# Optimization experiments

Measured on AMD Instinct MI355X. Metric: run time of the kernel, lower is better.

## Reference

```python
import jax, jax.numpy as jnp
import numpy as np

B, N, D_MODEL = 8, 1024, 512
H, DK = 8, 64
STATIONS = 128
MASK_NEG = -1e9
LN_EPS = 1e-6


def setup_inputs() -> dict:
    key = jax.random.key(0)
    ks = jax.random.split(key, 9)
    return {
        "hidden_states": jax.random.normal(ks[0], (B, N, D_MODEL), dtype=jnp.float32),
        "rpe": jax.random.normal(ks[1], (B, H, N, N), dtype=jnp.float32) * 0.1,
        "Wq": jax.random.normal(ks[2], (H * DK, D_MODEL), dtype=jnp.float32) * 0.02,
        "Wk": jax.random.normal(ks[3], (H * DK, D_MODEL), dtype=jnp.float32) * 0.02,
        "Wv": jax.random.normal(ks[4], (H * DK, D_MODEL), dtype=jnp.float32) * 0.02,
        "fc_w": jax.random.normal(ks[5], (D_MODEL, H * DK), dtype=jnp.float32) * 0.02,
        "fc_b": jnp.zeros((D_MODEL,), dtype=jnp.float32),
        "ln_g": jnp.ones((D_MODEL,), dtype=jnp.float32),
        "ln_b": jnp.zeros((D_MODEL,), dtype=jnp.float32),
    }


def _star_mask(n, stations):
    # q_k_mask: query i attends to key j iff j < stations or i == j
    idx = jnp.arange(n)
    return (idx[None, :] < stations) | (idx[:, None] == idx[None, :])  # [n, n] bool


def reference(hidden_states, rpe, Wq, Wk, Wv, fc_w, fc_b, ln_g, ln_b):
    b, n, _ = hidden_states.shape
    residual = hidden_states
    q = (hidden_states @ Wq.T).reshape(b, n, H, DK)
    k = (hidden_states @ Wk.T).reshape(b, n, H, DK)
    v = (hidden_states @ Wv.T).reshape(b, n, H, DK)
    # sparse star+self-loop QK^T with inline RPE add (dense emulation of QKP_mm_tvm)
    scores = jnp.einsum("bihd,bjhd->bhij", q, k) + rpe  # [b,h,n,n]
    mask = _star_mask(n, STATIONS)
    scores = jnp.where(mask[None, None], scores, MASK_NEG)
    scores = scores / jnp.sqrt(jnp.float32(DK))
    attn = jax.nn.softmax(scores, axis=-1)
    # AttnV_mm_tvm: sparse attn-weights times V
    ctx = jnp.einsum("bhij,bjhd->bihd", attn, v).reshape(b, n, H * DK)
    ctx = ctx @ fc_w.T + fc_b + residual
    mu = jnp.mean(ctx, axis=-1, keepdims=True)
    var = jnp.var(ctx, axis=-1, keepdims=True)
    return (ctx - mu) / jnp.sqrt(var + LN_EPS) * ln_g + ln_b
```

## Files before the change

kernel.cpp:

```cpp
#include <hip/hip_runtime.h>
#include <hip/hip_bf16.h>
#include <math.h>

#define B_  8
#define N_  1024
#define DM  512
#define H_  8
#define DK_ 64
#define ST  128

typedef __attribute__((ext_vector_type(8))) short short8;
typedef __attribute__((ext_vector_type(4))) float floatx4;

#define GLD16(gp, lp)                                                          \
    __builtin_amdgcn_global_load_lds(                                          \
        (const __attribute__((address_space(1))) void*)(gp),                   \
        (__attribute__((address_space(3))) void*)(lp), 16, 0, 0)

__device__ __forceinline__ float b2f(short u) {
    union { unsigned int i; float f; } c;
    c.i = ((unsigned int)(unsigned short)u) << 16;
    return c.f;
}
__device__ __forceinline__ unsigned short f2b(float f) {
    __hip_bfloat16 t = __float2bfloat16(f);
    return *(unsigned short*)&t;
}

struct CastArgs {
    const float* src[5];
    unsigned short* dst[5];
    int n[5];
};

__global__ __launch_bounds__(256)
void cast_bf16_kernel(CastArgs a)
{
    const int j = blockIdx.y;
    const float* __restrict__ s = a.src[j];
    unsigned short* __restrict__ d = a.dst[j];
    const int n = a.n[j];
    int i = (blockIdx.x * 256 + threadIdx.x) * 8;
    if (i >= n) return;
    float4 x0 = *(const float4*)&s[i];
    float4 x1 = *(const float4*)&s[i + 4];
    ushort4 o0, o1;
    o0.x = f2b(x0.x); o0.y = f2b(x0.y); o0.z = f2b(x0.z); o0.w = f2b(x0.w);
    o1.x = f2b(x1.x); o1.y = f2b(x1.y); o1.z = f2b(x1.z); o1.w = f2b(x1.w);
    *(ushort4*)&d[i] = o0;
    *(ushort4*)&d[i + 4] = o1;
}

__device__ __forceinline__
void gemm_core(const unsigned short* __restrict__ A,
               const unsigned short* __restrict__ W,
               int m0, int n0, unsigned short* As, unsigned short* Bs,
               floatx4 acc[4][4])
{
    const int tid = threadIdx.x;
    const int lane = tid & 63;
    const int wave = tid >> 6;
    const int wm = wave >> 1, wn = wave & 1;
    const int srow = tid >> 2;
    const int skq  = (tid & 3) * 8;
    const unsigned short* Ag = A + (size_t)(m0 + srow) * 512 + skq;
    const unsigned short* Bg = W + (size_t)(n0 + srow) * 512 + skq;
    const int mrow = lane & 15;
    const int koff = (lane >> 4) * 8;

    for (int kt = 0; kt < 512; kt += 32) {
        __syncthreads();
        GLD16(Ag + kt,            &As[tid * 8]);
        GLD16(Ag + 64 * 512 + kt, &As[2048 + tid * 8]);
        GLD16(Bg + kt,            &Bs[tid * 8]);
        GLD16(Bg + 64 * 512 + kt, &Bs[2048 + tid * 8]);
        __syncthreads();
        short8 af[4], bf[4];
        #pragma unroll
        for (int t = 0; t < 4; ++t) {
            af[t] = *(const short8*)&As[(wm * 64 + t * 16 + mrow) * 32 + koff];
            bf[t] = *(const short8*)&Bs[(wn * 64 + t * 16 + mrow) * 32 + koff];
        }
        #pragma unroll
        for (int mt = 0; mt < 4; ++mt)
            #pragma unroll
            for (int nt = 0; nt < 4; ++nt)
                acc[mt][nt] = __builtin_amdgcn_mfma_f32_16x16x32_bf16(
                    af[mt], bf[nt], acc[mt][nt], 0, 0, 0);
    }
}

__global__ __launch_bounds__(256)
void qkv_gemm_kernel(const unsigned short* __restrict__ A,
                     const unsigned short* __restrict__ W0,
                     const unsigned short* __restrict__ W1,
                     const unsigned short* __restrict__ W2,
                     unsigned short* __restrict__ qo,
                     unsigned short* __restrict__ ko,
                     unsigned short* __restrict__ vto)
{
    __shared__ __align__(16) unsigned short As[128 * 32];
    __shared__ __align__(16) unsigned short Bs[128 * 32];
    const int by = blockIdx.y;
    const int sel = by >> 2;
    const unsigned short* W = (sel == 0) ? W0 : (sel == 1 ? W1 : W2);
    const int m0 = blockIdx.x * 128;
    const int n0 = (by & 3) * 128;

    floatx4 acc[4][4];
    #pragma unroll
    for (int i = 0; i < 4; ++i)
        #pragma unroll
        for (int j = 0; j < 4; ++j)
            acc[i][j] = (floatx4){0.f, 0.f, 0.f, 0.f};

    gemm_core(A, W, m0, n0, As, Bs, acc);

    const int lane = threadIdx.x & 63;
    const int wave = threadIdx.x >> 6;
    const int wm = wave >> 1, wn = wave & 1;
    const int lx = lane & 15;
    const int rq = (lane >> 4) * 4;

    if (sel == 2) {
        #pragma unroll
        for (int mt = 0; mt < 4; ++mt) {
            const int mrow = m0 + wm * 64 + mt * 16 + rq;
            const int bb = mrow >> 10, tok = mrow & 1023;
            #pragma unroll
            for (int nt = 0; nt < 4; ++nt) {
                const int c = n0 + wn * 64 + nt * 16 + lx;
                const int hh = c >> 6, d = c & 63;
                ushort4 pk;
                pk.x = f2b(acc[mt][nt][0]); pk.y = f2b(acc[mt][nt][1]);
                pk.z = f2b(acc[mt][nt][2]); pk.w = f2b(acc[mt][nt][3]);
                *(ushort4*)&vto[((size_t)(bb * H_ + hh) * DK_ + d) * N_ + tok] = pk;
            }
        }
    } else {
        unsigned short* O = (sel == 0) ? qo : ko;
        #pragma unroll
        for (int mt = 0; mt < 4; ++mt) {
            const int mrow = m0 + wm * 64 + mt * 16 + rq;
            const int bb = mrow >> 10, tok = mrow & 1023;
            #pragma unroll
            for (int nt = 0; nt < 4; ++nt) {
                const int c = n0 + wn * 64 + nt * 16 + lx;
                const int hh = c >> 6, d = c & 63;
                unsigned short* p =
                    O + ((size_t)(bb * H_ + hh) * N_ + tok) * DK_ + d;
                #pragma unroll
                for (int r = 0; r < 4; ++r)
                    p[(size_t)r * DK_] = f2b(acc[mt][nt][r]);
            }
        }
    }
}

__global__ __launch_bounds__(256)
void attn_kernel(const unsigned short* __restrict__ qg,
                 const unsigned short* __restrict__ kg,
                 const unsigned short* __restrict__ vtg,
                 const float* __restrict__ rpe,
                 unsigned short* __restrict__ ctx)
{
    __shared__ __align__(16) unsigned short P[64 * 136];
    __shared__ __align__(16) unsigned short Vd[64 * 72];

    const int tid  = threadIdx.x;
    const int lane = tid & 63;
    const int w    = tid >> 6;
    const int lx   = lane & 15;
    const int quad = lane >> 4;
    const int qb = blockIdx.x * 64;
    const int h  = blockIdx.y, b = blockIdx.z;
    const int bh = b * H_ + h;
    const unsigned short* qh  = qg  + (size_t)bh * N_ * DK_;
    const unsigned short* kh  = kg  + (size_t)bh * N_ * DK_;
    const unsigned short* vth = vtg + (size_t)bh * DK_ * N_;
    const float* rp = rpe + ((size_t)bh * N_ + qb) * N_;
    const bool has_self = (qb >= ST);

    if (has_self) {
        const int d = tid >> 2, t16 = (tid & 3) * 16;
        const unsigned short* vs = vth + (size_t)d * N_ + qb + t16;
        *(short8*)&Vd[d * 72 + t16]     = *(const short8*)vs;
        *(short8*)&Vd[d * 72 + t16 + 8] = *(const short8*)(vs + 8);
    }

    float sself = -1e30f;
    if (has_self) {
        const int i = qb + w * 16 + lx;
        const unsigned short* qr = qh + (size_t)i * DK_ + quad * 16;
        const unsigned short* kr = kh + (size_t)i * DK_ + quad * 16;
        short8 q0 = *(const short8*)qr, q1 = *(const short8*)(qr + 8);
        short8 k0 = *(const short8*)kr, k1 = *(const short8*)(kr + 8);
        float dot = 0.f;
        #pragma unroll
        for (int j = 0; j < 8; ++j) {
            dot = fmaf(b2f(q0[j]), b2f(k0[j]), dot);
            dot = fmaf(b2f(q1[j]), b2f(k1[j]), dot);
        }
        dot += __shfl_xor(dot, 16, 64);
        dot += __shfl_xor(dot, 32, 64);
        const float rd = rp[(size_t)(w * 16 + lx) * N_ + (qb + w * 16 + lx)];
        sself = (dot + rd) * 0.125f;
    }

    float rv[4][8];
    {
        const float* rbase = rp + (size_t)(w * 16 + quad * 4) * N_ + lx;
        #pragma unroll
        for (int r = 0; r < 4; ++r)
            #pragma unroll
            for (int nt = 0; nt < 8; ++nt)
                rv[r][nt] = rbase[(size_t)r * N_ + nt * 16];
    }

    short8 aq[2];
    {
        const unsigned short* qrow =
            qh + (size_t)(qb + w * 16 + lx) * DK_ + quad * 8;
        aq[0] = *(const short8*)qrow;
        aq[1] = *(const short8*)(qrow + 32);
    }
    floatx4 sacc[8];
    #pragma unroll
    for (int nt = 0; nt < 8; ++nt) sacc[nt] = (floatx4){0.f, 0.f, 0.f, 0.f};
    #pragma unroll
    for (int nt = 0; nt < 8; ++nt) {
        const unsigned short* krow =
            kh + (size_t)(nt * 16 + lx) * DK_ + quad * 8;
        short8 b0 = *(const short8*)krow;
        short8 b1 = *(const short8*)(krow + 32);
        sacc[nt] = __builtin_amdgcn_mfma_f32_16x16x32_bf16(aq[0], b0, sacc[nt], 0, 0, 0);
        sacc[nt] = __builtin_amdgcn_mfma_f32_16x16x32_bf16(aq[1], b1, sacc[nt], 0, 0, 0);
    }

    float l4[4], ps4[4];
    #pragma unroll
    for (int r = 0; r < 4; ++r) {
        float sv[8];
        float mx = -1e30f;
        #pragma unroll
        for (int nt = 0; nt < 8; ++nt) {
            sv[nt] = (sacc[nt][r] + rv[r][nt]) * 0.125f;
            mx = fmaxf(mx, sv[nt]);
        }
        #pragma unroll
        for (int o = 1; o < 16; o <<= 1)
            mx = fmaxf(mx, __shfl_xor(mx, o, 64));
        const float ss = __shfl(sself, quad * 4 + r, 64);
        mx = fmaxf(mx, ss);
        float sum = 0.f;
        #pragma unroll
        for (int nt = 0; nt < 8; ++nt) {
            sv[nt] = __expf(sv[nt] - mx);
            sum += sv[nt];
        }
        #pragma unroll
        for (int o = 1; o < 16; o <<= 1)
            sum += __shfl_xor(sum, o, 64);
        const float ps = has_self ? __expf(ss - mx) : 0.f;
        l4[r] = sum + ps;
        ps4[r] = ps;
        const int row = w * 16 + quad * 4 + r;
        #pragma unroll
        for (int nt = 0; nt < 8; ++nt)
            P[row * 136 + nt * 16 + lx] = f2b(sv[nt]);
    }
    __syncthreads();

    short8 ap[4];
    #pragma unroll
    for (int ks = 0; ks < 4; ++ks)
        ap[ks] = *(const short8*)&P[(w * 16 + lx) * 136 + ks * 32 + quad * 8];
    floatx4 oacc[4];
    #pragma unroll
    for (int nt = 0; nt < 4; ++nt) oacc[nt] = (floatx4){0.f, 0.f, 0.f, 0.f};
    #pragma unroll
    for (int nt = 0; nt < 4; ++nt) {
        const unsigned short* vrow = vth + (size_t)(nt * 16 + lx) * N_;
        #pragma unroll
        for (int ks = 0; ks < 4; ++ks) {
            short8 bv = *(const short8*)(vrow + ks * 32 + quad * 8);
            oacc[nt] = __builtin_amdgcn_mfma_f32_16x16x32_bf16(ap[ks], bv, oacc[nt], 0, 0, 0);
        }
    }

    #pragma unroll
    for (int r = 0; r < 4; ++r) {
        const int il = w * 16 + quad * 4 + r;
        const int i = qb + il;
        const float inv = 1.0f / l4[r];
        const float ps = ps4[r];
        #pragma unroll
        for (int nt = 0; nt < 4; ++nt) {
            const int d = nt * 16 + lx;
            float o = oacc[nt][r];
            if (has_self)
                o = fmaf(ps, b2f((short)Vd[d * 72 + il]), o);
            ctx[((size_t)(b * N_) + i) * DM + h * DK_ + d] = f2b(o * inv);
        }
    }
}

__global__ __launch_bounds__(512)
void fc_ln_kernel(const unsigned short* __restrict__ A,
                  const unsigned short* __restrict__ W,
                  const float* __restrict__ bias,
                  const float* __restrict__ resid,
                  const float* __restrict__ g,
                  const float* __restrict__ bb,
                  float* __restrict__ out)
{
    __shared__ __align__(16) unsigned short As[32 * 32];
    __shared__ __align__(16) unsigned short Bs[512 * 32];
    __shared__ float lsum[32][8];
    __shared__ float lsq[32][8];

    const int tid  = threadIdx.x;
    const int lane = tid & 63;
    const int wv   = tid >> 6;
    const int m0   = blockIdx.x * 32;

    const int srow = tid >> 2;
    const int skq  = (tid & 3) * 8;
    const unsigned short* Ag = A + (size_t)(m0 + srow) * 512 + skq;
    const unsigned short* Bg = W + (size_t)srow * 512 + skq;

    const int mrow = lane & 15;
    const int koff = (lane >> 4) * 8;

    floatx4 acc[2][4];
    #pragma unroll
    for (int i = 0; i < 2; ++i)
        #pragma unroll
        for (int j = 0; j < 4; ++j)
            acc[i][j] = (floatx4){0.f, 0.f, 0.f, 0.f};

    for (int kt = 0; kt < 512; kt += 32) {
        __syncthreads();
        if (tid < 128)
            GLD16(Ag + kt, &As[tid * 8]);
        #pragma unroll
        for (int p = 0; p < 4; ++p)
            GLD16(Bg + (size_t)p * 128 * 512 + kt, &Bs[p * 4096 + tid * 8]);
        __syncthreads();
        short8 af[2], bf[4];
        #pragma unroll
        for (int t = 0; t < 2; ++t)
            af[t] = *(const short8*)&As[(t * 16 + mrow) * 32 + koff];
        #pragma unroll
        for (int t = 0; t < 4; ++t)
            bf[t] = *(const short8*)&Bs[(wv * 64 + t * 16 + mrow) * 32 + koff];
        #pragma unroll
        for (int mt = 0; mt < 2; ++mt)
            #pragma unroll
            for (int nt = 0; nt < 4; ++nt)
                acc[mt][nt] = __builtin_amdgcn_mfma_f32_16x16x32_bf16(
                    af[mt], bf[nt], acc[mt][nt], 0, 0, 0);
    }

    const int quad = lane >> 4;
    const int lx   = lane & 15;
    float s[2][4], ss[2][4];
    #pragma unroll
    for (int mt = 0; mt < 2; ++mt)
        #pragma unroll
        for (int r = 0; r < 4; ++r) { s[mt][r] = 0.f; ss[mt][r] = 0.f; }

    #pragma unroll
    for (int mt = 0; mt < 2; ++mt)
        #pragma unroll
        for (int nt = 0; nt < 4; ++nt) {
            const int c = wv * 64 + nt * 16 + lx;
            const float bvv = bias[c];
            #pragma unroll
            for (int r = 0; r < 4; ++r) {
                const size_t row = (size_t)(m0 + mt * 16 + quad * 4 + r);
                float v = acc[mt][nt][r] + bvv + resid[row * 512 + c];
                acc[mt][nt][r] = v;
                s[mt][r] += v;
                ss[mt][r] = fmaf(v, v, ss[mt][r]);
            }
        }

    #pragma unroll
    for (int o = 1; o < 16; o <<= 1)
        #pragma unroll
        for (int mt = 0; mt < 2; ++mt)
            #pragma unroll
            for (int r = 0; r < 4; ++r) {
                s[mt][r]  += __shfl_xor(s[mt][r],  o, 64);
                ss[mt][r] += __shfl_xor(ss[mt][r], o, 64);
            }
    if (lx == 0) {
        #pragma unroll
        for (int mt = 0; mt < 2; ++mt)
            #pragma unroll
            for (int r = 0; r < 4; ++r) {
                lsum[mt * 16 + quad * 4 + r][wv] = s[mt][r];
                lsq [mt * 16 + quad * 4 + r][wv] = ss[mt][r];
            }
    }
    __syncthreads();

    #pragma unroll
    for (int mt = 0; mt < 2; ++mt)
        #pragma unroll
        for (int r = 0; r < 4; ++r) {
            const int rl = mt * 16 + quad * 4 + r;
            float ts = 0.f, tss = 0.f;
            #pragma unroll
            for (int u = 0; u < 8; ++u) { ts += lsum[rl][u]; tss += lsq[rl][u]; }
            const float mean = ts * (1.0f / DM);
            const float var  = tss * (1.0f / DM) - mean * mean;
            const float rstd = rsqrtf(var + 1e-6f);
            const size_t row = (size_t)(m0 + rl);
            #pragma unroll
            for (int nt = 0; nt < 4; ++nt) {
                const int c = wv * 64 + nt * 16 + lx;
                out[row * 512 + c] =
                    (acc[mt][nt][r] - mean) * rstd * g[c] + bb[c];
            }
        }
}

extern "C" void kernel_launch(void* const* d_in, const int* in_sizes, int n_in,
                              void* d_out, int out_size, void* d_ws, size_t ws_size,
                              hipStream_t stream)
{
    (void)in_sizes; (void)n_in; (void)out_size; (void)ws_size;
    const float* hidden = (const float*)d_in[0];
    const float* rpe    = (const float*)d_in[1];
    const float* Wq     = (const float*)d_in[2];
    const float* Wk     = (const float*)d_in[3];
    const float* Wv     = (const float*)d_in[4];
    const float* fc_w   = (const float*)d_in[5];
    const float* fc_b   = (const float*)d_in[6];
    const float* ln_g   = (const float*)d_in[7];
    const float* ln_b   = (const float*)d_in[8];
    float* out = (float*)d_out;
    char* ws = (char*)d_ws;

    const size_t MB = 1024 * 1024;
    unsigned short* hb  = (unsigned short*)(ws + 0 * MB);
    unsigned short* wq  = (unsigned short*)(ws + 8 * MB);
    unsigned short* wk  = (unsigned short*)(ws + 8 * MB + 512 * 1024);
    unsigned short* wv  = (unsigned short*)(ws + 9 * MB);
    unsigned short* wf  = (unsigned short*)(ws + 9 * MB + 512 * 1024);
    unsigned short* qB  = (unsigned short*)(ws + 16 * MB);
    unsigned short* kB  = (unsigned short*)(ws + 24 * MB);
    unsigned short* vtB = (unsigned short*)(ws + 32 * MB);
    unsigned short* cb  = (unsigned short*)(ws + 40 * MB);

    CastArgs ca;
    ca.src[0] = hidden; ca.dst[0] = hb; ca.n[0] = B_ * N_ * DM;
    ca.src[1] = Wq;     ca.dst[1] = wq; ca.n[1] = DM * DM;
    ca.src[2] = Wk;     ca.dst[2] = wk; ca.n[2] = DM * DM;
    ca.src[3] = Wv;     ca.dst[3] = wv; ca.n[3] = DM * DM;
    ca.src[4] = fc_w;   ca.dst[4] = wf; ca.n[4] = DM * DM;
    cast_bf16_kernel<<<dim3(2048, 5), 256, 0, stream>>>(ca);

    qkv_gemm_kernel<<<dim3(64, 12), 256, 0, stream>>>(hb, wq, wk, wv, qB, kB, vtB);
    attn_kernel<<<dim3(16, H_, B_), 256, 0, stream>>>(qB, kB, vtB, rpe, cb);
    fc_ln_kernel<<<dim3(256), 512, 0, stream>>>(cb, wf, fc_b, hidden, ln_g, ln_b, out);
}
```

Before: 390.1 us.

## Double-buffer LDS tiles in QKV and FC GEMMs; compact cast grid

The QKV and FC+LayerNorm GEMM main loops now use two LDS buffers, so the async global-to-LDS load for the next K slice is issued before the MFMA work on the current slice. This aims to hide global load latency and halves the number of barriers per K step. The cast kernel's grid is also flattened so that no blocks are launched only to exit early for the small weight tensors. Doubling LDS use, about 64KB for the FC kernel, may reduce occupancy.

```diff
diff --git a/kernel.cpp b/kernel.cpp
--- a/kernel.cpp
+++ b/kernel.cpp
@@ -30,18 +30,18 @@
 struct CastArgs {
     const float* src[5];
     unsigned short* dst[5];
-    int n[5];
 };
 
 __global__ __launch_bounds__(256)
 void cast_bf16_kernel(CastArgs a)
 {
-    const int j = blockIdx.y;
+    const int bx = blockIdx.x;
+    int j, base;
+    if (bx < 2048) { j = 0; base = bx; }
+    else { const int r = bx - 2048; j = 1 + (r >> 7); base = r & 127; }
     const float* __restrict__ s = a.src[j];
     unsigned short* __restrict__ d = a.dst[j];
-    const int n = a.n[j];
-    int i = (blockIdx.x * 256 + threadIdx.x) * 8;
-    if (i >= n) return;
+    const int i = (base * 256 + threadIdx.x) * 8;
     float4 x0 = *(const float4*)&s[i];
     float4 x1 = *(const float4*)&s[i + 4];
     ushort4 o0, o1;
@@ -49,6 +49,24 @@
     o1.x = f2b(x1.x); o1.y = f2b(x1.y); o1.z = f2b(x1.z); o1.w = f2b(x1.w);
     *(ushort4*)&d[i] = o0;
     *(ushort4*)&d[i + 4] = o1;
+}
+
+__device__ __forceinline__
+void gemm_step(const unsigned short* Ac, const unsigned short* Bc,
+               int wm, int wn, int mrow, int koff, floatx4 acc[4][4])
+{
+    short8 af[4], bf[4];
+    #pragma unroll
+    for (int t = 0; t < 4; ++t) {
+        af[t] = *(const short8*)&Ac[(wm * 64 + t * 16 + mrow) * 32 + koff];
+        bf[t] = *(const short8*)&Bc[(wn * 64 + t * 16 + mrow) * 32 + koff];
+    }
+    #pragma unroll
+    for (int mt = 0; mt < 4; ++mt)
+        #pragma unroll
+        for (int nt = 0; nt < 4; ++nt)
+            acc[mt][nt] = __builtin_amdgcn_mfma_f32_16x16x32_bf16(
+                af[mt], bf[nt], acc[mt][nt], 0, 0, 0);
 }
 
 __device__ __forceinline__
@@ -68,26 +86,31 @@
     const int mrow = lane & 15;
     const int koff = (lane >> 4) * 8;
 
-    for (int kt = 0; kt < 512; kt += 32) {
+    unsigned short* A0 = As;        unsigned short* A1 = As + 4096;
+    unsigned short* B0 = Bs;        unsigned short* B1 = Bs + 4096;
+
+#define STAGE4(Ad, Bd, off)                                                    \
+    do {                                                                       \
+        GLD16(Ag + (off),            &(Ad)[tid * 8]);                          \
+        GLD16(Ag + 64 * 512 + (off), &(Ad)[2048 + tid * 8]);                   \
+        GLD16(Bg + (off),            &(Bd)[tid * 8]);                          \
+        GLD16(Bg + 64 * 512 + (off), &(Bd)[2048 + tid * 8]);                   \
+    } while (0)
+
+    STAGE4(A0, B0, 0);
+    __syncthreads();
+
+    #pragma unroll
+    for (int kt = 0; kt < 512; kt += 64) {
+        STAGE4(A1, B1, kt + 32);
+        gemm_step(A0, B0, wm, wn, mrow, koff, acc);
         __syncthreads();
-        GLD16(Ag + kt,            &As[tid * 8]);
-        GLD16(Ag + 64 * 512 + kt, &As[2048 + tid * 8]);
-        GLD16(Bg + kt,            &Bs[tid * 8]);
-        GLD16(Bg + 64 * 512 + kt, &Bs[2048 + tid * 8]);
+        if (kt + 64 < 512)
+            STAGE4(A0, B0, kt + 64);
+        gemm_step(A1, B1, wm, wn, mrow, koff, acc);
         __syncthreads();
-        short8 af[4], bf[4];
-        #pragma unroll
-        for (int t = 0; t < 4; ++t) {
-            af[t] = *(const short8*)&As[(wm * 64 + t * 16 + mrow) * 32 + koff];
-            bf[t] = *(const short8*)&Bs[(wn * 64 + t * 16 + mrow) * 32 + koff];
-        }
-        #pragma unroll
-        for (int mt = 0; mt < 4; ++mt)
-            #pragma unroll
-            for (int nt = 0; nt < 4; ++nt)
-                acc[mt][nt] = __builtin_amdgcn_mfma_f32_16x16x32_bf16(
-                    af[mt], bf[nt], acc[mt][nt], 0, 0, 0);
-    }
+    }
+#undef STAGE4
 }
 
 __global__ __launch_bounds__(256)
@@ -99,8 +122,8 @@
                      unsigned short* __restrict__ ko,
                      unsigned short* __restrict__ vto)
 {
-    __shared__ __align__(16) unsigned short As[128 * 32];
-    __shared__ __align__(16) unsigned short Bs[128 * 32];
+    __shared__ __align__(16) unsigned short As[2 * 128 * 32];
+    __shared__ __align__(16) unsigned short Bs[2 * 128 * 32];
     const int by = blockIdx.y;
     const int sel = by >> 2;
     const unsigned short* W = (sel == 0) ? W0 : (sel == 1 ? W1 : W2);
@@ -305,6 +328,25 @@
     }
 }
 
+__device__ __forceinline__
+void fc_step(const unsigned short* Ac, const unsigned short* Bc,
+             int wv, int mrow, int koff, floatx4 acc[2][4])
+{
+    short8 af[2], bf[4];
+    #pragma unroll
+    for (int t = 0; t < 2; ++t)
+        af[t] = *(const short8*)&Ac[(t * 16 + mrow) * 32 + koff];
+    #pragma unroll
+    for (int t = 0; t < 4; ++t)
+        bf[t] = *(const short8*)&Bc[(wv * 64 + t * 16 + mrow) * 32 + koff];
+    #pragma unroll
+    for (int mt = 0; mt < 2; ++mt)
+        #pragma unroll
+        for (int nt = 0; nt < 4; ++nt)
+            acc[mt][nt] = __builtin_amdgcn_mfma_f32_16x16x32_bf16(
+                af[mt], bf[nt], acc[mt][nt], 0, 0, 0);
+}
+
 __global__ __launch_bounds__(512)
 void fc_ln_kernel(const unsigned short* __restrict__ A,
                   const unsigned short* __restrict__ W,
@@ -314,8 +356,8 @@
                   const float* __restrict__ bb,
                   float* __restrict__ out)
 {
-    __shared__ __align__(16) unsigned short As[32 * 32];
-    __shared__ __align__(16) unsigned short Bs[512 * 32];
+    __shared__ __align__(16) unsigned short As[2 * 32 * 32];
+    __shared__ __align__(16) unsigned short Bs[2 * 512 * 32];
     __shared__ float lsum[32][8];
     __shared__ float lsq[32][8];
 
@@ -332,6 +374,18 @@
     const int mrow = lane & 15;
     const int koff = (lane >> 4) * 8;
 
+    unsigned short* A0 = As;        unsigned short* A1 = As + 1024;
+    unsigned short* B0 = Bs;        unsigned short* B1 = Bs + 16384;
+
+#define FSTAGE(Ad, Bd, off)                                                    \
+    do {                                                                       \
+        if (tid < 128) GLD16(Ag + (off), &(Ad)[tid * 8]);                      \
+        _Pragma("unroll")                                                      \
+        for (int p = 0; p < 4; ++p)                                            \
+            GLD16(Bg + (size_t)p * 128 * 512 + (off),                          \
+                  &(Bd)[p * 4096 + tid * 8]);                                  \
+    } while (0)
+
     floatx4 acc[2][4];
     #pragma unroll
     for (int i = 0; i < 2; ++i)
@@ -339,28 +393,20 @@
         for (int j = 0; j < 4; ++j)
             acc[i][j] = (floatx4){0.f, 0.f, 0.f, 0.f};
 
-    for (int kt = 0; kt < 512; kt += 32) {
+    FSTAGE(A0, B0, 0);
+    __syncthreads();
+
+    #pragma unroll
+    for (int kt = 0; kt < 512; kt += 64) {
+        FSTAGE(A1, B1, kt + 32);
+        fc_step(A0, B0, wv, mrow, koff, acc);
         __syncthreads();
-        if (tid < 128)
-            GLD16(Ag + kt, &As[tid * 8]);
-        #pragma unroll
-        for (int p = 0; p < 4; ++p)
-            GLD16(Bg + (size_t)p * 128 * 512 + kt, &Bs[p * 4096 + tid * 8]);
+        if (kt + 64 < 512)
+            FSTAGE(A0, B0, kt + 64);
+        fc_step(A1, B1, wv, mrow, koff, acc);
         __syncthreads();
-        short8 af[2], bf[4];
-        #pragma unroll
-        for (int t = 0; t < 2; ++t)
-            af[t] = *(const short8*)&As[(t * 16 + mrow) * 32 + koff];
-        #pragma unroll
-        for (int t = 0; t < 4; ++t)
-            bf[t] = *(const short8*)&Bs[(wv * 64 + t * 16 + mrow) * 32 + koff];
-        #pragma unroll
-        for (int mt = 0; mt < 2; ++mt)
-            #pragma unroll
-            for (int nt = 0; nt < 4; ++nt)
-                acc[mt][nt] = __builtin_amdgcn_mfma_f32_16x16x32_bf16(
-                    af[mt], bf[nt], acc[mt][nt], 0, 0, 0);
-    }
+    }
+#undef FSTAGE
 
     const int quad = lane >> 4;
     const int lx   = lane & 15;
@@ -456,12 +502,12 @@
     unsigned short* cb  = (unsigned short*)(ws + 40 * MB);
 
     CastArgs ca;
-    ca.src[0] = hidden; ca.dst[0] = hb; ca.n[0] = B_ * N_ * DM;
-    ca.src[1] = Wq;     ca.dst[1] = wq; ca.n[1] = DM * DM;
-    ca.src[2] = Wk;     ca.dst[2] = wk; ca.n[2] = DM * DM;
-    ca.src[3] = Wv;     ca.dst[3] = wv; ca.n[3] = DM * DM;
-    ca.src[4] = fc_w;   ca.dst[4] = wf; ca.n[4] = DM * DM;
-    cast_bf16_kernel<<<dim3(2048, 5), 256, 0, stream>>>(ca);
+    ca.src[0] = hidden; ca.dst[0] = hb;
+    ca.src[1] = Wq;     ca.dst[1] = wq;
+    ca.src[2] = Wk;     ca.dst[2] = wk;
+    ca.src[3] = Wv;     ca.dst[3] = wv;
+    ca.src[4] = fc_w;   ca.dst[4] = wf;
+    cast_bf16_kernel<<<dim3(2048 + 4 * 128), 256, 0, stream>>>(ca);
 
     qkv_gemm_kernel<<<dim3(64, 12), 256, 0, stream>>>(hb, wq, wk, wv, qB, kB, vtB);
     attn_kernel<<<dim3(16, H_, B_), 256, 0, stream>>>(qB, kB, vtB, rpe, cb);
```

Measured after the change: 390.2 us. About the same (+0.0%).

## Widen GEMM K-tile to 64 with XOR-swizzled LDS and compact cast grid

Applied to the files above, without the earlier changes.

Both the QKV GEMM and the FC+LayerNorm GEMM now stage 64-wide K slices per iteration instead of 32. This halves the number of barrier pairs, and the LDS layout uses an XOR swizzle to avoid bank conflicts on the short8 fragment reads. The cast kernel launch drops the mostly-idle blocks of the 2048x5 grid by mapping a flat 1D grid onto the five tensors. The cost is more LDS per block: the fc_ln kernel grows to about 68KB, which may reduce occupancy.

```diff
diff --git a/kernel.cpp b/kernel.cpp
--- a/kernel.cpp
+++ b/kernel.cpp
@@ -30,18 +30,18 @@
 struct CastArgs {
     const float* src[5];
     unsigned short* dst[5];
-    int n[5];
 };
 
 __global__ __launch_bounds__(256)
 void cast_bf16_kernel(CastArgs a)
 {
-    const int j = blockIdx.y;
+    const int bx = blockIdx.x;
+    int j, base;
+    if (bx < 2048) { j = 0; base = bx; }
+    else { const int r = bx - 2048; j = 1 + (r >> 7); base = r & 127; }
     const float* __restrict__ s = a.src[j];
     unsigned short* __restrict__ d = a.dst[j];
-    const int n = a.n[j];
-    int i = (blockIdx.x * 256 + threadIdx.x) * 8;
-    if (i >= n) return;
+    const int i = (base * 256 + threadIdx.x) * 8;
     float4 x0 = *(const float4*)&s[i];
     float4 x1 = *(const float4*)&s[i + 4];
     ushort4 o0, o1;
@@ -57,36 +57,43 @@
                int m0, int n0, unsigned short* As, unsigned short* Bs,
                floatx4 acc[4][4])
 {
-    const int tid = threadIdx.x;
+    const int tid  = threadIdx.x;
     const int lane = tid & 63;
     const int wave = tid >> 6;
     const int wm = wave >> 1, wn = wave & 1;
-    const int srow = tid >> 2;
-    const int skq  = (tid & 3) * 8;
+    const int srow = tid >> 3;
+    const int skq  = (((tid >> 3) ^ tid) & 7) * 8;
     const unsigned short* Ag = A + (size_t)(m0 + srow) * 512 + skq;
     const unsigned short* Bg = W + (size_t)(n0 + srow) * 512 + skq;
     const int mrow = lane & 15;
     const int koff = (lane >> 4) * 8;
-
-    for (int kt = 0; kt < 512; kt += 32) {
+    const int sx   = (lane & 7) * 8;
+
+    for (int kt = 0; kt < 512; kt += 64) {
         __syncthreads();
-        GLD16(Ag + kt,            &As[tid * 8]);
-        GLD16(Ag + 64 * 512 + kt, &As[2048 + tid * 8]);
-        GLD16(Bg + kt,            &Bs[tid * 8]);
-        GLD16(Bg + 64 * 512 + kt, &Bs[2048 + tid * 8]);
+        #pragma unroll
+        for (int r = 0; r < 4; ++r) {
+            GLD16(Ag + (size_t)r * 32 * 512 + kt, &As[r * 2048 + tid * 8]);
+            GLD16(Bg + (size_t)r * 32 * 512 + kt, &Bs[r * 2048 + tid * 8]);
+        }
         __syncthreads();
-        short8 af[4], bf[4];
-        #pragma unroll
-        for (int t = 0; t < 4; ++t) {
-            af[t] = *(const short8*)&As[(wm * 64 + t * 16 + mrow) * 32 + koff];
-            bf[t] = *(const short8*)&Bs[(wn * 64 + t * 16 + mrow) * 32 + koff];
-        }
-        #pragma unroll
-        for (int mt = 0; mt < 4; ++mt)
-            #pragma unroll
-            for (int nt = 0; nt < 4; ++nt)
-                acc[mt][nt] = __builtin_amdgcn_mfma_f32_16x16x32_bf16(
-                    af[mt], bf[nt], acc[mt][nt], 0, 0, 0);
+        #pragma unroll
+        for (int kk = 0; kk < 2; ++kk) {
+            short8 af[4], bf[4];
+            #pragma unroll
+            for (int t = 0; t < 4; ++t) {
+                af[t] = *(const short8*)
+                    &As[((wm * 64 + t * 16 + mrow) * 64 + kk * 32 + koff) ^ sx];
+                bf[t] = *(const short8*)
+                    &Bs[((wn * 64 + t * 16 + mrow) * 64 + kk * 32 + koff) ^ sx];
+            }
+            #pragma unroll
+            for (int mt = 0; mt < 4; ++mt)
+                #pragma unroll
+                for (int nt = 0; nt < 4; ++nt)
+                    acc[mt][nt] = __builtin_amdgcn_mfma_f32_16x16x32_bf16(
+                        af[mt], bf[nt], acc[mt][nt], 0, 0, 0);
+        }
     }
 }
 
@@ -99,8 +106,8 @@
                      unsigned short* __restrict__ ko,
                      unsigned short* __restrict__ vto)
 {
-    __shared__ __align__(16) unsigned short As[128 * 32];
-    __shared__ __align__(16) unsigned short Bs[128 * 32];
+    __shared__ __align__(16) unsigned short As[128 * 64];
+    __shared__ __align__(16) unsigned short Bs[128 * 64];
     const int by = blockIdx.y;
     const int sel = by >> 2;
     const unsigned short* W = (sel == 0) ? W0 : (sel == 1 ? W1 : W2);
@@ -314,8 +321,8 @@
                   const float* __restrict__ bb,
                   float* __restrict__ out)
 {
-    __shared__ __align__(16) unsigned short As[32 * 32];
-    __shared__ __align__(16) unsigned short Bs[512 * 32];
+    __shared__ __align__(16) unsigned short As[32 * 64];
+    __shared__ __align__(16) unsigned short Bs[512 * 64];
     __shared__ float lsum[32][8];
     __shared__ float lsq[32][8];
 
@@ -324,13 +331,14 @@
     const int wv   = tid >> 6;
     const int m0   = blockIdx.x * 32;
 
-    const int srow = tid >> 2;
-    const int skq  = (tid & 3) * 8;
-    const unsigned short* Ag = A + (size_t)(m0 + srow) * 512 + skq;
+    const int srow = tid >> 3;
+    const int skq  = (((tid >> 3) ^ tid) & 7) * 8;
+    const unsigned short* Ag = A + (size_t)(m0 + (srow & 31)) * 512 + skq;
     const unsigned short* Bg = W + (size_t)srow * 512 + skq;
 
     const int mrow = lane & 15;
     const int koff = (lane >> 4) * 8;
+    const int sx   = (lane & 7) * 8;
 
     floatx4 acc[2][4];
     #pragma unroll
@@ -339,27 +347,32 @@
         for (int j = 0; j < 4; ++j)
             acc[i][j] = (floatx4){0.f, 0.f, 0.f, 0.f};
 
-    for (int kt = 0; kt < 512; kt += 32) {
+    for (int kt = 0; kt < 512; kt += 64) {
         __syncthreads();
-        if (tid < 128)
+        if (tid < 256)
             GLD16(Ag + kt, &As[tid * 8]);
         #pragma unroll
-        for (int p = 0; p < 4; ++p)
-            GLD16(Bg + (size_t)p * 128 * 512 + kt, &Bs[p * 4096 + tid * 8]);
+        for (int r = 0; r < 8; ++r)
+            GLD16(Bg + (size_t)r * 64 * 512 + kt, &Bs[r * 4096 + tid * 8]);
         __syncthreads();
-        short8 af[2], bf[4];
-        #pragma unroll
-        for (int t = 0; t < 2; ++t)
-            af[t] = *(const short8*)&As[(t * 16 + mrow) * 32 + koff];
-        #pragma unroll
-        for (int t = 0; t < 4; ++t)
-            bf[t] = *(const short8*)&Bs[(wv * 64 + t * 16 + mrow) * 32 + koff];
-        #pragma unroll
-        for (int mt = 0; mt < 2; ++mt)
-            #pragma unroll
-            for (int nt = 0; nt < 4; ++nt)
-                acc[mt][nt] = __builtin_amdgcn_mfma_f32_16x16x32_bf16(
-                    af[mt], bf[nt], acc[mt][nt], 0, 0, 0);
+        #pragma unroll
+        for (int kk = 0; kk < 2; ++kk) {
+            short8 af[2], bf[4];
+            #pragma unroll
+            for (int t = 0; t < 2; ++t)
+                af[t] = *(const short8*)
+                    &As[((t * 16 + mrow) * 64 + kk * 32 + koff) ^ sx];
+            #pragma unroll
+            for (int t = 0; t < 4; ++t)
+                bf[t] = *(const short8*)
+                    &Bs[((wv * 64 + t * 16 + mrow) * 64 + kk * 32 + koff) ^ sx];
+            #pragma unroll
+            for (int mt = 0; mt < 2; ++mt)
+                #pragma unroll
+                for (int nt = 0; nt < 4; ++nt)
+                    acc[mt][nt] = __builtin_amdgcn_mfma_f32_16x16x32_bf16(
+                        af[mt], bf[nt], acc[mt][nt], 0, 0, 0);
+        }
     }
 
     const int quad = lane >> 4;
@@ -456,12 +469,12 @@
     unsigned short* cb  = (unsigned short*)(ws + 40 * MB);
 
     CastArgs ca;
-    ca.src[0] = hidden; ca.dst[0] = hb; ca.n[0] = B_ * N_ * DM;
-    ca.src[1] = Wq;     ca.dst[1] = wq; ca.n[1] = DM * DM;
-    ca.src[2] = Wk;     ca.dst[2] = wk; ca.n[2] = DM * DM;
-    ca.src[3] = Wv;     ca.dst[3] = wv; ca.n[3] = DM * DM;
-    ca.src[4] = fc_w;   ca.dst[4] = wf; ca.n[4] = DM * DM;
-    cast_bf16_kernel<<<dim3(2048, 5), 256, 0, stream>>>(ca);
+    ca.src[0] = hidden; ca.dst[0] = hb;
+    ca.src[1] = Wq;     ca.dst[1] = wq;
+    ca.src[2] = Wk;     ca.dst[2] = wk;
+    ca.src[3] = Wv;     ca.dst[3] = wv;
+    ca.src[4] = fc_w;   ca.dst[4] = wf;
+    cast_bf16_kernel<<<dim3(2048 + 4 * 128), 256, 0, stream>>>(ca);
 
     qkv_gemm_kernel<<<dim3(64, 12), 256, 0, stream>>>(hb, wq, wk, wv, qB, kB, vtB);
     attn_kernel<<<dim3(16, H_, B_), 256, 0, stream>>>(qB, kB, vtB, rpe, cb);
```

New measurement: 387.1 us. No clear change (-0.8%).
